# Optimization experiments

Hardware: AMD Instinct MI355X
Metric: run time of the kernel (lower is better)

The kernel has to match this reference:

```python
import jax, jax.numpy as jnp
import numpy as np

HEADS = 8
HEAD_DIM = 64
SCALE = HEAD_DIM ** -0.5


def setup_inputs() -> dict:
    key = jax.random.key(0)
    ks = jax.random.split(key, 5)
    d_model, inner = 1024, HEADS * HEAD_DIM  # 512
    x = jax.random.normal(ks[0], (2, 2048, d_model), dtype=jnp.float32)
    # torch Linear weights stored pre-transposed as [in, out]
    Wq = jax.random.normal(ks[1], (d_model, inner), dtype=jnp.float32) * (d_model ** -0.5)
    Wkv = jax.random.normal(ks[2], (d_model, 2 * inner), dtype=jnp.float32) * (d_model ** -0.5)
    Wo = jax.random.normal(ks[3], (inner, d_model), dtype=jnp.float32) * (inner ** -0.5)
    bo = jnp.zeros((d_model,), dtype=jnp.float32)
    return {"x": x, "Wq": Wq, "Wkv": Wkv, "Wo": Wo, "bo": bo}


def reference(x, Wq, Wkv, Wo, bo):
    b, n, _ = x.shape
    q = x @ Wq                       # [b, n, h*d]
    kv = x @ Wkv                     # [b, n, 2*h*d] (self-attention: context = x)
    k, v = jnp.split(kv, 2, axis=-1)

    def split_heads(t):
        return t.reshape(b, n, HEADS, HEAD_DIM).transpose(0, 2, 1, 3)  # [b, h, n, d]

    q, k, v = map(split_heads, (q, k, v))
    sim = jnp.einsum('bhid,bhjd->bhij', q, k) * SCALE  # [b, h, n, n]
    attn = jax.nn.softmax(sim, axis=-1)                # dropout p=0.0 -> identity
    out = jnp.einsum('bhij,bhjd->bhid', attn, v)       # [b, h, n, d]
    out = out.transpose(0, 2, 1, 3).reshape(b, n, HEADS * HEAD_DIM)
    return out @ Wo + bo
```

## Files before the change

### kernel.cpp

```cpp
#include <hip/hip_runtime.h>

typedef _Float16 f16;
typedef __attribute__((ext_vector_type(4))) _Float16 f16x4;
typedef __attribute__((ext_vector_type(8))) _Float16 f16x8;
typedef __attribute__((ext_vector_type(4))) float f32x4;

#define CEXP 0.18033688011112042f
#define QKB_LD 1056
#define FIXM 12.0f

__device__ __forceinline__ void gload16(const f16* g, f16* l) {
    __builtin_amdgcn_global_load_lds((const __attribute__((address_space(1))) void*)g,
                                     (__attribute__((address_space(3))) void*)l, 16, 0, 0);
}

__global__ __launch_bounds__(256) void prep_k(const float* __restrict__ x,
                                              const float* __restrict__ Wq,
                                              const float* __restrict__ Wkv,
                                              const float* __restrict__ Wo,
                                              f16* __restrict__ xb,
                                              f16* __restrict__ wqkvT,
                                              f16* __restrict__ woT) {
    int z = blockIdx.z;
    if (z == 3) {
        size_t idx = ((size_t)(blockIdx.y * 32 + blockIdx.x) * 256 + threadIdx.x) * 16;
#pragma unroll
        for (int h = 0; h < 2; h++) {
            float4 a = *(const float4*)(x + idx + h * 8);
            float4 b = *(const float4*)(x + idx + h * 8 + 4);
            f16x8 o;
            o[0] = (f16)a.x; o[1] = (f16)a.y; o[2] = (f16)a.z; o[3] = (f16)a.w;
            o[4] = (f16)b.x; o[5] = (f16)b.y; o[6] = (f16)b.z; o[7] = (f16)b.w;
            *(f16x8*)(xb + idx + h * 8) = o;
        }
        return;
    }
    const float* in; f16* out; int N, ldo, row_off, gx, gy;
    if (z == 0)      { in = Wq;  out = wqkvT; N = 512;  ldo = 1024; row_off = 0;   gx = 16; gy = 32; }
    else if (z == 1) { in = Wkv; out = wqkvT; N = 1024; ldo = 1024; row_off = 512; gx = 32; gy = 32; }
    else             { in = Wo;  out = woT;   N = 1024; ldo = 512;  row_off = 0;   gx = 32; gy = 16; }
    if (blockIdx.x >= gx || blockIdx.y >= gy) return;

    __shared__ float tile[32][33];
    int tx = threadIdx.x & 31, ty = threadIdx.x >> 5;
    int n0 = blockIdx.x * 32, k0 = blockIdx.y * 32;
#pragma unroll
    for (int j = 0; j < 4; j++)
        tile[ty + j * 8][tx] = in[(size_t)(k0 + ty + j * 8) * N + n0 + tx];
    __syncthreads();
#pragma unroll
    for (int j = 0; j < 4; j++)
        out[(size_t)(row_off + n0 + ty + j * 8) * ldo + k0 + tx] = (f16)tile[tx][ty + j * 8];
}

template <int MODE, int BN>
__global__ __launch_bounds__(256) void gemm_k(
    const f16* __restrict__ A, const f16* __restrict__ Bt,
    f16* __restrict__ Cqk, f16* __restrict__ Cvt,
    float* __restrict__ Cout, const float* __restrict__ bias,
    int K, int NTILES) {
    __shared__ __align__(16) f16 As[2][128 * 64];
    __shared__ __align__(16) f16 Bs[2][BN * 64];
    constexpr int MI = (BN == 128) ? 4 : 2;
    constexpr int NB = (BN == 128) ? 4 : 2;
    int bid = blockIdx.x;
    int nt = bid % NTILES, mt = bid / NTILES;
    int m0 = mt * 128, n0 = nt * BN;
    int tid = threadIdx.x;
    int lane = tid & 63, w = tid >> 6;
    int rowBase = (BN == 128) ? (w >> 1) * 64 : w * 32;
    int colBase = (BN == 128) ? (w & 1) * 64 : 0;
    int lr = lane & 15, lg = lane >> 4;
    int rowL = lane >> 3;
    int colL = (lane & 7) * 8;
    int bRow0 = (BN == 128) ? w * 32 : w * 16;
    const f16* aSrc = A + (size_t)(m0 + w * 32 + rowL) * K + colL;
    const f16* bSrc = Bt + (size_t)(n0 + bRow0 + rowL) * K + colL;
    f32x4 acc[MI][4] = {};

    auto stage = [&](int buf, int k0) {
#pragma unroll
        for (int j = 0; j < 4; j++)
            gload16(aSrc + k0 + (size_t)(j * 8) * K, &As[buf][(w * 32 + j * 8) * 64]);
#pragma unroll
        for (int j = 0; j < NB; j++)
            gload16(bSrc + k0 + (size_t)(j * 8) * K, &Bs[buf][(bRow0 + j * 8) * 64]);
    };

    stage(0, 0);
    __syncthreads();

    int KT = K >> 6;
    for (int kt = 0; kt < KT; kt++) {
        int cur = kt & 1;
        if (kt + 1 < KT) stage(cur ^ 1, (kt + 1) * 64);
#pragma unroll
        for (int ks = 0; ks < 2; ks++) {
            f16x8 af[MI], bf[4];
#pragma unroll
            for (int i = 0; i < MI; i++)
                af[i] = *(const f16x8*)(&As[cur][(rowBase + i * 16 + lr) * 64 + ks * 32 + lg * 8]);
#pragma unroll
            for (int j = 0; j < 4; j++)
                bf[j] = *(const f16x8*)(&Bs[cur][(colBase + j * 16 + lr) * 64 + ks * 32 + lg * 8]);
#pragma unroll
            for (int i = 0; i < MI; i++)
#pragma unroll
                for (int j = 0; j < 4; j++)
                    acc[i][j] = __builtin_amdgcn_mfma_f32_16x16x32_f16(af[i], bf[j], acc[i][j], 0, 0, 0);
        }
        __syncthreads();
    }

#pragma unroll
    for (int i = 0; i < MI; i++) {
#pragma unroll
        for (int j = 0; j < 4; j++) {
            int row = m0 + rowBase + i * 16 + lg * 4;
            int col = n0 + colBase + j * 16 + lr;
            if (MODE == 1) {
                float bv = bias[col];
#pragma unroll
                for (int r = 0; r < 4; r++)
                    Cout[(size_t)(row + r) * 1024 + col] = acc[i][j][r] + bv;
            } else {
                if (col < 1024) {
                    float sc = (col < 512) ? CEXP : 1.0f;
#pragma unroll
                    for (int r = 0; r < 4; r++)
                        Cqk[(size_t)(row + r) * QKB_LD + col] = (f16)(acc[i][j][r] * sc);
                } else {
                    int c = col - 1024;
                    int hh = c >> 6, d = c & 63;
                    int bb = row >> 11, n = row & 2047;
                    int pr = bb * 8 + hh;
                    int tt = n >> 6, kvl = n & 63;
                    int kg = kvl >> 4, lga = (kvl >> 2) & 3;
                    int dgp = d >> 5, dh = (d >> 4) & 1, lra = d & 15;
                    f16x4 ov;
#pragma unroll
                    for (int r = 0; r < 4; r++) ov[r] = (f16)acc[i][j][r];
                    size_t idx = ((((size_t)(pr * 32 + tt) * 4 + kg) * 2 + dgp) * 64
                                  + lga * 16 + lra) * 8 + dh * 4;
                    *(f16x4*)(Cvt + idx) = ov;
                }
            }
        }
    }
}

__global__ __launch_bounds__(256, 4) void attn_k(const f16* __restrict__ qkb,
                                                 const f16* __restrict__ vt2,
                                                 f16* __restrict__ ao) {
    __shared__ __align__(16) f16 Ks[2][2][64 * 64];

    int bid = blockIdx.x;
    int xcd = bid & 7;
    int pair = xcd * 2 + ((bid >> 3) & 1);
    int qblk = bid >> 4;
    int b = pair >> 3, h = pair & 7;
    int tid = threadIdx.x;
    int lane = tid & 63, w = tid >> 6;
    int half = w >> 1, wl = w & 1;
    int lr = lane & 15, lg = lane >> 4;
    int q0 = qblk * 32 + wl * 16;

    const f16* qb = qkb + (size_t)b * 2048 * QKB_LD + h * 64;
    const f16* kb = qb + 512;

    f16x8 qf0 = *(const f16x8*)(qb + (size_t)(q0 + lr) * QKB_LD + lg * 8);
    f16x8 qf1 = *(const f16x8*)(qb + (size_t)(q0 + lr) * QKB_LD + 32 + lg * 8);

    int srcCol = (((lane & 7) ^ (lane >> 3)) << 3);
    int rowL = lane >> 3;
    const f16* ksrc = kb + (size_t)(half * 1024 + wl * 32 + rowL) * QKB_LD + srcCol;
    const f16* vbase = vt2 + ((size_t)pair * 32) * 4096 + lane * 8;

    auto stageK = [&](int buf, int tt) {
        f16* dst = &Ks[half][buf][(wl * 32) * 64];
        const f16* s = ksrc + (size_t)(tt * 64) * QKB_LD;
#pragma unroll
        for (int j = 0; j < 4; j++)
            gload16(s + (size_t)(j * 8) * QKB_LD, dst + (j * 8) * 64);
    };

    stageK(0, 0);
    __syncthreads();

    int kOffA = (lg * 8) ^ ((lr & 7) << 3);

    f32x4 acc[4] = {};
    float lp = 0.f;

    for (int t = 0; t < 16; t++) {
        int cur = t & 1;

        const f16* vl = vbase + (size_t)(half * 16 + t) * 4096;
        f16x8 vv[8];
#pragma unroll
        for (int i = 0; i < 8; i++) vv[i] = *(const f16x8*)(vl + i * 512);

        if (t < 15) stageK(cur ^ 1, t + 1);

        __builtin_amdgcn_s_setprio(1);
#pragma unroll
        for (int kg = 0; kg < 4; kg++) {
            const f16* krow = &Ks[half][cur][(kg * 16 + lr) * 64];
            f16x8 ka0 = *(const f16x8*)(krow + kOffA);
            f16x8 ka1 = *(const f16x8*)(krow + (kOffA ^ 32));
            f32x4 z = {};
            z = __builtin_amdgcn_mfma_f32_16x16x32_f16(ka0, qf0, z, 0, 0, 0);
            f32x4 s = __builtin_amdgcn_mfma_f32_16x16x32_f16(ka1, qf1, z, 0, 0, 0);

            float p0 = __builtin_amdgcn_exp2f(s[0] - FIXM);
            float p1 = __builtin_amdgcn_exp2f(s[1] - FIXM);
            float p2 = __builtin_amdgcn_exp2f(s[2] - FIXM);
            float p3 = __builtin_amdgcn_exp2f(s[3] - FIXM);
            lp += (p0 + p1) + (p2 + p3);
            f16x4 pf;
            pf[0] = (f16)p0; pf[1] = (f16)p1; pf[2] = (f16)p2; pf[3] = (f16)p3;

            f16x8 vx0 = vv[kg * 2], vx1 = vv[kg * 2 + 1];
            f16x4 v0lo = __builtin_shufflevector(vx0, vx0, 0, 1, 2, 3);
            f16x4 v0hi = __builtin_shufflevector(vx0, vx0, 4, 5, 6, 7);
            f16x4 v1lo = __builtin_shufflevector(vx1, vx1, 0, 1, 2, 3);
            f16x4 v1hi = __builtin_shufflevector(vx1, vx1, 4, 5, 6, 7);
            acc[0] = __builtin_amdgcn_mfma_f32_16x16x16f16(v0lo, pf, acc[0], 0, 0, 0);
            acc[1] = __builtin_amdgcn_mfma_f32_16x16x16f16(v0hi, pf, acc[1], 0, 0, 0);
            acc[2] = __builtin_amdgcn_mfma_f32_16x16x16f16(v1lo, pf, acc[2], 0, 0, 0);
            acc[3] = __builtin_amdgcn_mfma_f32_16x16x16f16(v1hi, pf, acc[3], 0, 0, 0);
        }
        __builtin_amdgcn_s_setprio(0);

        if (t < 15) __syncthreads();
    }

    lp += __shfl_xor(lp, 16, 64);
    lp += __shfl_xor(lp, 32, 64);
    __syncthreads();
    float* mO = (float*)&Ks[0][0][0];
    float* mL = mO + 2 * 64 * 16;
    if (half == 1) {
#pragma unroll
        for (int dg = 0; dg < 4; dg++)
            *(f32x4*)&mO[(wl * 64 + lane) * 16 + dg * 4] = acc[dg];
        mL[wl * 64 + lane] = lp;
    }
    __syncthreads();
    if (half == 0) {
        float inv = 1.f / (lp + mL[wl * 64 + lane]);
#pragma unroll
        for (int dg = 0; dg < 4; dg++) {
            f32x4 oP = *(const f32x4*)&mO[(wl * 64 + lane) * 16 + dg * 4];
            f16x4 ov;
#pragma unroll
            for (int r = 0; r < 4; r++)
                ov[r] = (f16)((acc[dg][r] + oP[r]) * inv);
            *(f16x4*)(ao + (size_t)(b * 2048 + q0 + lr) * 512 + h * 64 + dg * 16 + lg * 4) = ov;
        }
    }
}

extern "C" void kernel_launch(void* const* d_in, const int* in_sizes, int n_in,
                              void* d_out, int out_size, void* d_ws, size_t ws_size,
                              hipStream_t stream) {
    const float* x   = (const float*)d_in[0];
    const float* Wq  = (const float*)d_in[1];
    const float* Wkv = (const float*)d_in[2];
    const float* Wo  = (const float*)d_in[3];
    const float* bo  = (const float*)d_in[4];
    float* out = (float*)d_out;

    f16* xb    = (f16*)d_ws;
    f16* wqkvT = xb + 4096 * 1024;
    f16* woT   = wqkvT + 1536 * 1024;
    f16* qkb   = woT + 1024 * 512;
    f16* vtb2  = qkb + 4096 * QKB_LD;
    f16* ao    = vtb2 + 16 * 32 * 4096;

    prep_k<<<dim3(32, 32, 4), 256, 0, stream>>>(x, Wq, Wkv, Wo, xb, wqkvT, woT);
    gemm_k<0, 64><<<32 * 24, 256, 0, stream>>>(xb, wqkvT, qkb, vtb2, nullptr, nullptr, 1024, 24);
    attn_k<<<1024, 256, 0, stream>>>(qkb, vtb2, ao);
    gemm_k<1, 128><<<32 * 8, 256, 0, stream>>>(ao, woT, nullptr, nullptr, out, bo, 512, 8);
}
```

Baseline: 87.76 us.

## Pre-swizzle K into MFMA fragment layout and load directly to registers

The QKV GEMM epilogue now writes K in a fragment-ordered layout, like V already was, and stores Q in its own narrower buffer. The attention kernel drops the LDS double-buffered K staging and its per-tile barriers. Instead it loads K and V fragments straight from global memory into registers, prefetching the next tile between the QK and PV phases. This removes LDS traffic and synchronisation, at the cost of more registers per thread, scattered 2-byte stores in the GEMM epilogue, and reliance on L2 reuse across blocks.

Result: no change. 89.26 us (+1.7%).

```diff
diff --git a/kernel.cpp b/kernel.cpp
--- a/kernel.cpp
+++ b/kernel.cpp
@@ -6,7 +6,7 @@
 typedef __attribute__((ext_vector_type(4))) float f32x4;
 
 #define CEXP 0.18033688011112042f
-#define QKB_LD 1056
+#define QB_LD 544
 #define FIXM 12.0f
 
 __device__ __forceinline__ void gload16(const f16* g, f16* l) {
@@ -56,7 +56,7 @@
 template <int MODE, int BN>
 __global__ __launch_bounds__(256) void gemm_k(
     const f16* __restrict__ A, const f16* __restrict__ Bt,
-    f16* __restrict__ Cqk, f16* __restrict__ Cvt,
+    f16* __restrict__ Cq, f16* __restrict__ Ckf, f16* __restrict__ Cvt,
     float* __restrict__ Cout, const float* __restrict__ bias,
     int K, int NTILES) {
     __shared__ __align__(16) f16 As[2][128 * 64];
@@ -124,11 +124,23 @@
                 for (int r = 0; r < 4; r++)
                     Cout[(size_t)(row + r) * 1024 + col] = acc[i][j][r] + bv;
             } else {
-                if (col < 1024) {
-                    float sc = (col < 512) ? CEXP : 1.0f;
+                if (col < 512) {
 #pragma unroll
                     for (int r = 0; r < 4; r++)
-                        Cqk[(size_t)(row + r) * QKB_LD + col] = (f16)(acc[i][j][r] * sc);
+                        Cq[(size_t)(row + r) * QB_LD + col] = (f16)(acc[i][j][r] * CEXP);
+                } else if (col < 1024) {
+                    int c2 = col - 512;
+                    int hh = c2 >> 6, d = c2 & 63;
+                    int pair = (row >> 11) * 8 + hh;
+                    int n = row & 2047;
+                    int t = n >> 6, kvl = n & 63;
+                    int kg = kvl >> 4, lrA = kvl & 15;
+                    int cc = d >> 5, lgA = (d >> 3) & 3, j8 = d & 7;
+                    size_t base = ((((size_t)(pair * 32 + t) * 4 + kg) * 2 + cc) * 64
+                                   + lgA * 16 + lrA) * 8 + j8;
+#pragma unroll
+                    for (int r = 0; r < 4; r++)
+                        Ckf[base + r * 8] = (f16)acc[i][j][r];
                 } else {
                     int c = col - 1024;
                     int hh = c >> 6, d = c & 63;
@@ -149,10 +161,12 @@
     }
 }
 
-__global__ __launch_bounds__(256, 4) void attn_k(const f16* __restrict__ qkb,
+__global__ __launch_bounds__(256, 4) void attn_k(const f16* __restrict__ qb2,
+                                                 const f16* __restrict__ kfb,
                                                  const f16* __restrict__ vt2,
                                                  f16* __restrict__ ao) {
-    __shared__ __align__(16) f16 Ks[2][2][64 * 64];
+    __shared__ float mO[2][64][16];
+    __shared__ float mL[2][64];
 
     int bid = blockIdx.x;
     int xcd = bid & 7;
@@ -165,57 +179,54 @@
     int lr = lane & 15, lg = lane >> 4;
     int q0 = qblk * 32 + wl * 16;
 
-    const f16* qb = qkb + (size_t)b * 2048 * QKB_LD + h * 64;
-    const f16* kb = qb + 512;
-
-    f16x8 qf0 = *(const f16x8*)(qb + (size_t)(q0 + lr) * QKB_LD + lg * 8);
-    f16x8 qf1 = *(const f16x8*)(qb + (size_t)(q0 + lr) * QKB_LD + 32 + lg * 8);
-
-    int srcCol = (((lane & 7) ^ (lane >> 3)) << 3);
-    int rowL = lane >> 3;
-    const f16* ksrc = kb + (size_t)(half * 1024 + wl * 32 + rowL) * QKB_LD + srcCol;
+    const f16* qrow = qb2 + ((size_t)b * 2048 + q0 + lr) * QB_LD + h * 64;
+    f16x8 qf0 = *(const f16x8*)(qrow + lg * 8);
+    f16x8 qf1 = *(const f16x8*)(qrow + 32 + lg * 8);
+
+    const f16* kbase = kfb + ((size_t)pair * 32) * 4096 + lane * 8;
     const f16* vbase = vt2 + ((size_t)pair * 32) * 4096 + lane * 8;
-
-    auto stageK = [&](int buf, int tt) {
-        f16* dst = &Ks[half][buf][(wl * 32) * 64];
-        const f16* s = ksrc + (size_t)(tt * 64) * QKB_LD;
-#pragma unroll
-        for (int j = 0; j < 4; j++)
-            gload16(s + (size_t)(j * 8) * QKB_LD, dst + (j * 8) * 64);
-    };
-
-    stageK(0, 0);
-    __syncthreads();
-
-    int kOffA = (lg * 8) ^ ((lr & 7) << 3);
+    int tg0 = half * 16;
+
+    f16x8 kk[8], vv[8];
+    {
+        const f16* kp = kbase + (size_t)tg0 * 4096;
+        const f16* vp = vbase + (size_t)tg0 * 4096;
+#pragma unroll
+        for (int u = 0; u < 8; u++) kk[u] = *(const f16x8*)(kp + u * 512);
+#pragma unroll
+        for (int u = 0; u < 8; u++) vv[u] = *(const f16x8*)(vp + u * 512);
+    }
 
     f32x4 acc[4] = {};
     float lp = 0.f;
 
+#pragma unroll 1
     for (int t = 0; t < 16; t++) {
-        int cur = t & 1;
-
-        const f16* vl = vbase + (size_t)(half * 16 + t) * 4096;
-        f16x8 vv[8];
-#pragma unroll
-        for (int i = 0; i < 8; i++) vv[i] = *(const f16x8*)(vl + i * 512);
-
-        if (t < 15) stageK(cur ^ 1, t + 1);
-
+        int tn = tg0 + ((t < 15) ? t + 1 : t);
+
+        f32x4 s[4];
         __builtin_amdgcn_s_setprio(1);
 #pragma unroll
         for (int kg = 0; kg < 4; kg++) {
-            const f16* krow = &Ks[half][cur][(kg * 16 + lr) * 64];
-            f16x8 ka0 = *(const f16x8*)(krow + kOffA);
-            f16x8 ka1 = *(const f16x8*)(krow + (kOffA ^ 32));
             f32x4 z = {};
-            z = __builtin_amdgcn_mfma_f32_16x16x32_f16(ka0, qf0, z, 0, 0, 0);
-            f32x4 s = __builtin_amdgcn_mfma_f32_16x16x32_f16(ka1, qf1, z, 0, 0, 0);
-
-            float p0 = __builtin_amdgcn_exp2f(s[0] - FIXM);
-            float p1 = __builtin_amdgcn_exp2f(s[1] - FIXM);
-            float p2 = __builtin_amdgcn_exp2f(s[2] - FIXM);
-            float p3 = __builtin_amdgcn_exp2f(s[3] - FIXM);
+            z = __builtin_amdgcn_mfma_f32_16x16x32_f16(kk[kg * 2], qf0, z, 0, 0, 0);
+            s[kg] = __builtin_amdgcn_mfma_f32_16x16x32_f16(kk[kg * 2 + 1], qf1, z, 0, 0, 0);
+        }
+        __builtin_amdgcn_s_setprio(0);
+
+        {
+            const f16* kp = kbase + (size_t)tn * 4096;
+#pragma unroll
+            for (int u = 0; u < 8; u++) kk[u] = *(const f16x8*)(kp + u * 512);
+        }
+
+        __builtin_amdgcn_s_setprio(1);
+#pragma unroll
+        for (int kg = 0; kg < 4; kg++) {
+            float p0 = __builtin_amdgcn_exp2f(s[kg][0] - FIXM);
+            float p1 = __builtin_amdgcn_exp2f(s[kg][1] - FIXM);
+            float p2 = __builtin_amdgcn_exp2f(s[kg][2] - FIXM);
+            float p3 = __builtin_amdgcn_exp2f(s[kg][3] - FIXM);
             lp += (p0 + p1) + (p2 + p3);
             f16x4 pf;
             pf[0] = (f16)p0; pf[1] = (f16)p1; pf[2] = (f16)p2; pf[3] = (f16)p3;
@@ -232,26 +243,27 @@
         }
         __builtin_amdgcn_s_setprio(0);
 
-        if (t < 15) __syncthreads();
+        {
+            const f16* vp = vbase + (size_t)tn * 4096;
+#pragma unroll
+            for (int u = 0; u < 8; u++) vv[u] = *(const f16x8*)(vp + u * 512);
+        }
     }
 
     lp += __shfl_xor(lp, 16, 64);
     lp += __shfl_xor(lp, 32, 64);
-    __syncthreads();
-    float* mO = (float*)&Ks[0][0][0];
-    float* mL = mO + 2 * 64 * 16;
     if (half == 1) {
 #pragma unroll
         for (int dg = 0; dg < 4; dg++)
-            *(f32x4*)&mO[(wl * 64 + lane) * 16 + dg * 4] = acc[dg];
-        mL[wl * 64 + lane] = lp;
+            *(f32x4*)&mO[wl][lane][dg * 4] = acc[dg];
+        mL[wl][lane] = lp;
     }
     __syncthreads();
     if (half == 0) {
-        float inv = 1.f / (lp + mL[wl * 64 + lane]);
+        float inv = 1.f / (lp + mL[wl][lane]);
 #pragma unroll
         for (int dg = 0; dg < 4; dg++) {
-            f32x4 oP = *(const f32x4*)&mO[(wl * 64 + lane) * 16 + dg * 4];
+            f32x4 oP = *(const f32x4*)&mO[wl][lane][dg * 4];
             f16x4 ov;
 #pragma unroll
             for (int r = 0; r < 4; r++)
@@ -274,12 +286,13 @@
     f16* xb    = (f16*)d_ws;
     f16* wqkvT = xb + 4096 * 1024;
     f16* woT   = wqkvT + 1536 * 1024;
-    f16* qkb   = woT + 1024 * 512;
-    f16* vtb2  = qkb + 4096 * QKB_LD;
+    f16* qb2   = woT + 1024 * 512;
+    f16* kfb   = qb2 + 4096 * QB_LD;
+    f16* vtb2  = kfb + 16 * 32 * 4096;
     f16* ao    = vtb2 + 16 * 32 * 4096;
 
     prep_k<<<dim3(32, 32, 4), 256, 0, stream>>>(x, Wq, Wkv, Wo, xb, wqkvT, woT);
-    gemm_k<0, 64><<<32 * 24, 256, 0, stream>>>(xb, wqkvT, qkb, vtb2, nullptr, nullptr, 1024, 24);
-    attn_k<<<1024, 256, 0, stream>>>(qkb, vtb2, ao);
-    gemm_k<1, 128><<<32 * 8, 256, 0, stream>>>(ao, woT, nullptr, nullptr, out, bo, 512, 8);
-}
+    gemm_k<0, 64><<<32 * 24, 256, 0, stream>>>(xb, wqkvT, qb2, kfb, vtb2, nullptr, nullptr, 1024, 24);
+    attn_k<<<1024, 256, 0, stream>>>(qb2, kfb, vtb2, ao);
+    gemm_k<1, 128><<<32 * 8, 256, 0, stream>>>(ao, woT, nullptr, nullptr, nullptr, out, bo, 512, 8);
+}
```
